# Kernel tuning notes

Measured on AMD Instinct MI355X. Metric: run time of the kernel, lower is better.

## Reference

```python
import jax, jax.numpy as jnp
import numpy as np
from jax import lax

TAU = 2.0     # spikingjelly LIFNode default tau
ALPHA = 4.0   # sigmoid surrogate default alpha

@jax.custom_vjp
def spike(x):
    # heaviside: spikingjelly uses (x >= 0)
    return (x >= 0).astype(x.dtype)

def _spike_fwd(x):
    return spike(x), x

def _spike_bwd(x, g):
    s = jax.nn.sigmoid(ALPHA * x)
    return (g * ALPHA * s * (1.0 - s),)

spike.defvjp(_spike_fwd, _spike_bwd)

def lif(x_seq, v_th):
    """Multi-step LIF: v += (x - v)/tau (decay_input, v_reset=0); hard reset."""
    def step(v, xt):
        v = v + (xt - v) / TAU
        s = spike(v - v_th)
        return (1.0 - s) * v, s
    _, out = lax.scan(step, jnp.zeros_like(x_seq[0]), x_seq)
    return out  # [T,B,C,V] of {0,1}

def conv_bn(x, W, scale, shift):
    # 1x1 Conv1d (no bias) on [T,B,C,V] + eval-mode BatchNorm(s) fused to affine
    y = jnp.einsum('oc,tbcv->tbov', W, x)
    return y * scale[None, None, :, None] + shift[None, None, :, None]

def setup_inputs() -> dict:
    key = jax.random.key(0)
    ks = jax.random.split(key, 16)
    T, B, C, V = 4, 16, 512, 1024
    d = {"x": jax.random.normal(ks[0], (T, B, C, V), jnp.float32)}
    for i, n in enumerate(["q", "k", "v", "p"]):
        d[f"W{n}"] = jax.random.normal(ks[1 + i], (C, C), jnp.float32) * 0.02
        d[f"s{n}"] = 1.0 + 0.1 * jax.random.normal(ks[5 + i], (C,), jnp.float32)
        d[f"b{n}"] = 0.1 * jax.random.normal(ks[9 + i], (C,), jnp.float32)
    return d

def reference(x, Wq, sq, bq, Wk, sk, bk, Wv, sv, bv, Wp, sp, bp):
    T, B, C, V = x.shape
    H = 8
    dh = C // H
    attn_scale = 0.125

    xs = lif(x, 1.0)                              # head_lif, spikes in {0,1}
    q = lif(conv_bn(xs, Wq, sq, bq), 1.0)         # [T,B,C,V]
    k = lif(conv_bn(xs, Wk, sk, bk), 1.0)
    v = lif(conv_bn(xs, Wv, sv, bv), 1.0)

    def to_heads(t):
        # [T,B,C,V] -> [T,B,H,N,dh]  (N = V)
        return t.transpose(0, 1, 3, 2).reshape(T, B, V, H, dh).transpose(0, 1, 3, 2, 4)

    qh, kh, vh = to_heads(q), to_heads(k), to_heads(v)
    kv = jnp.einsum('tbhnd,tbhne->tbhde', kh, vh)            # [T,B,H,dh,dh]
    o = jnp.einsum('tbhnd,tbhde->tbhne', qh, kv) * attn_scale  # [T,B,H,N,dh]
    o = o.transpose(0, 1, 2, 4, 3).reshape(T, B, C, V)       # -> [T,B,C,N]

    a = lif(o, 0.5)                               # attn_lif, v_threshold=0.5
    return conv_bn(a, Wp, sp, bp)                 # [T,B,C,V]
```

## Files before the change

kernel.cpp:

```cpp
#include <hip/hip_runtime.h>
#include <stdint.h>

#define TT 4
#define BB 16
#define CC 512
#define VV 1024
#define OO 1536

typedef __attribute__((ext_vector_type(4)))  int      i32x4;
typedef __attribute__((ext_vector_type(4)))  float    f32x4;
typedef __attribute__((ext_vector_type(16))) uint8_t  u8x16;
typedef __attribute__((ext_vector_type(8)))  uint8_t  u8x8;
typedef __attribute__((ext_vector_type(8)))  int8_t   i8x8;

__device__ __forceinline__ float bf2f(unsigned short u){
  union { unsigned int i; float f; } x; x.i = ((unsigned int)u) << 16; return x.f;
}
__device__ __forceinline__ unsigned short f2bf(float f){
  union { float f; unsigned int i; } x; x.f = f;
  unsigned int u = x.i;
  return (unsigned short)((u + 0x7fffu + ((u >> 16) & 1u)) >> 16);
}

__device__ __forceinline__ void g2lds16(const void* g, void* l){
  __builtin_amdgcn_global_load_lds(
      (const __attribute__((address_space(1))) unsigned int*)g,
      (__attribute__((address_space(3))) unsigned int*)l,
      16, 0, 0);
}

__global__ __launch_bounds__(256) void k_head_lif_prep(
    const float* __restrict__ x, int8_t* __restrict__ xs8,
    const float* __restrict__ Wq, const float* __restrict__ sq, const float* __restrict__ bq,
    const float* __restrict__ Wk, const float* __restrict__ sk, const float* __restrict__ bk,
    const float* __restrict__ Wv, const float* __restrict__ sv, const float* __restrict__ bv,
    const float* __restrict__ Wp, const float* __restrict__ sp,
    int8_t* __restrict__ Wq8, float* __restrict__ scales, float* __restrict__ bias,
    unsigned short* __restrict__ WpT, int* __restrict__ flags)
{
  int bid = blockIdx.x;
  int tid = threadIdx.x;

  if (bid >= 2048) {
    if (bid < 2176) {
      int idx = bid - 2048;
      int lane = tid & 63, wvv = tid >> 6;
      if (idx == 0 && tid < 2) flags[tid] = 0;
      #pragma unroll
      for (int p = 0; p < 3; ++p) {
        int o = idx*12 + p*4 + wvv;
        const float *W, *s, *b; int oo;
        if (o < 512)       { W = Wq; s = sq; b = bq; oo = o; }
        else if (o < 1024) { W = Wk; s = sk; b = bk; oo = o - 512; }
        else               { W = Wv; s = sv; b = bv; oo = o - 1024; }
        float sv_ = s[oo];
        float w[8]; float amax = 0.f;
        #pragma unroll
        for (int j=0;j<8;j++){
          w[j] = W[oo*512 + lane*8 + j] * sv_;
          amax = fmaxf(amax, fabsf(w[j]));
        }
        #pragma unroll
        for (int off=32; off; off>>=1) amax = fmaxf(amax, __shfl_xor(amax, off));
        float scale = (amax > 0.f) ? amax*(1.f/127.f) : 1.f;
        float inv = 1.f/scale;
        i8x8 q;
        #pragma unroll
        for (int j=0;j<8;j++){
          int qi = (int)rintf(w[j]*inv);
          qi = qi > 127 ? 127 : (qi < -127 ? -127 : qi);
          q[j] = (int8_t)qi;
        }
        *(i8x8*)(Wq8 + o*512 + lane*8) = q;
        if (lane == 0){ scales[o] = scale; bias[o] = b[oo]; }
      }
    } else {
      int j0 = (bid - 2176)*1024 + tid*4;
      #pragma unroll
      for (int i=0;i<4;i++){
        int j = j0 + i; int o = j >> 9, c = j & 511;
        WpT[c*512 + o] = f2bf(Wp[j]*sp[o]);
      }
    }
    return;
  }

  int vt = bid & 15, ct = (bid >> 4) & 7, b = bid >> 7;
  int c0 = ct*64, v0 = vt*64;
  __shared__ uint8_t sp_[64][68];
  int cr = tid >> 4;
  int vr = tid & 15;
  float st[4][4];
  #pragma unroll
  for (int i=0;i<4;i++) for (int j=0;j<4;j++) st[i][j]=0.f;
  for (int t=0;t<TT;t++){
    size_t tb = (size_t)t*BB + b;
    const float* xt = x + (tb*CC + c0) * (size_t)VV + v0;
    #pragma unroll
    for (int i=0;i<4;i++){
      const float4 xv = *(const float4*)(xt + (size_t)(cr + i*16)*VV + vr*4);
      const float xe[4] = {xv.x, xv.y, xv.z, xv.w};
      #pragma unroll
      for (int j=0;j<4;j++){
        float vv = st[i][j];
        vv = vv + (xe[j] - vv) * 0.5f;
        bool s = (vv >= 1.0f);
        sp_[cr + i*16][vr*4 + j] = s ? 1 : 0;
        st[i][j] = s ? 0.f : vv;
      }
    }
    __syncthreads();
    int v_loc = tid >> 2;
    int c16 = (tid & 3) * 16;
    u8x16 o0;
    #pragma unroll
    for (int j=0;j<16;j++) o0[j] = sp_[c16 + j][v_loc];
    *(u8x16*)(xs8 + (tb*VV + v0 + v_loc)*(size_t)CC + c0 + c16) = o0;
    __syncthreads();
  }
}

template<int STORE>
__global__ __launch_bounds__(256, 2) void k_gemm_fused(
    const int8_t* __restrict__ xs8, const int8_t* __restrict__ Wq8,
    const float* __restrict__ scales, const float* __restrict__ bias,
    const float* __restrict__ bp, float* __restrict__ outp,
    uint8_t* __restrict__ spk, int* __restrict__ flags)
{
  if (STORE && flags[0] == 0) return;
  int orig = blockIdx.x;
  int tid = threadIdx.x, lane = tid & 63, wv = tid >> 6;

  float bvv = 0.f;
  if (!STORE) bvv = bp[orig & 511];

  int wg = (orig >> 3) + (orig & 7) * 192;
  int ot = wg % 12;
  int r  = wg / 12;
  int vt = r & 7;
  int b  = r >> 3;
  int o0 = ot*128, v0 = vt*128;

  __shared__ __attribute__((aligned(16))) uint8_t lds[81920];

  int wm = wv >> 1, wn = wv & 1;

  const int8_t* Bg = Wq8 + (size_t)o0 * CC;

  {
    int orl = lane >> 5;
    int sl  = lane & 31;
    #pragma unroll
    for (int i=0;i<16;i++){
      int j = wv*16 + i;
      int orow = j*2 + orl;
      int c16 = sl ^ (orow & 7);
      g2lds16(Bg + (size_t)orow*CC + (c16 << 4), lds + j*1024);
    }
  }

  auto STAGE_A = [&](int buf, const int8_t* base, int k0){
    int rl  = lane >> 2;
    int c16 = (lane & 3) ^ ((lane >> 3) & 3);
    #pragma unroll
    for (int i=0;i<2;i++){
      int j = wv*2 + i;
      g2lds16(base + (size_t)(j*16 + rl)*CC + k0 + (c16 << 4),
              lds + 65536 + buf*8192 + j*1024);
    }
  };
  auto READB = [&](int ks, i32x4* dst){
    #pragma unroll
    for (int n=0;n<4;n++){
      int orow = wn*64 + n*16 + (lane & 15);
      int slot = (((ks & 7) << 2) + (lane >> 4)) ^ (lane & 7);
      dst[n] = *(const i32x4*)(lds + orow*512 + (slot << 4));
    }
  };

  i32x4 acc[4][4];
  float st[4][4][4];
  #pragma unroll
  for (int m=0;m<4;m++)
    #pragma unroll
    for (int n=0;n<4;n++){
      acc[m][n] = (i32x4){0,0,0,0};
      #pragma unroll
      for (int j=0;j<4;j++) st[m][n][j] = 0.f;
    }

  float sc[4], bi[4];
  #pragma unroll
  for (int n=0;n<4;n++){
    int og = o0 + wn*64 + n*16 + (lane & 15);
    sc[n] = scales[og];
    bi[n] = bias[og];
  }

  const int8_t* A0 = xs8 + ((size_t)b*VV + v0) * CC;
  STAGE_A(0, A0, 0);

  int anyspike = 0;
  for (int t=0; t<TT; ++t){
    const int8_t* At = xs8 + ((size_t)(t*BB + b)*VV + v0) * CC;
    const int8_t* An = xs8 + ((size_t)((t+1)*BB + b)*VV + v0) * CC;
    #pragma unroll
    for (int ks=0; ks<8; ++ks){
      int g = t*8 + ks;
      int cur = ks & 1;

      if (STORE) {
        __syncthreads();
      } else {
        asm volatile("s_waitcnt vmcnt(0)" ::: "memory");
        __builtin_amdgcn_s_barrier();
      }

      if (!STORE && g < 21) {
        size_t R = (size_t)g*1536 + orig;
        f32x4 val = (f32x4){bvv, bvv, bvv, bvv};
        __builtin_nontemporal_store(val, (f32x4*)(outp + R*1024 + tid*4));
      }

      if (ks < 7)          STAGE_A(cur^1, At, (ks+1)*64);
      else if (t < TT-1)   STAGE_A(cur^1, An, 0);

      const uint8_t* bufA = lds + 65536 + cur*8192;
      i32x4 af[4], bfr[4];
      #pragma unroll
      for (int m=0;m<4;m++){
        int rr = wm*64 + m*16 + (lane & 15);
        int slot = (lane >> 4) ^ ((lane >> 1) & 3);
        af[m] = *(const i32x4*)(bufA + rr*64 + (slot << 4));
      }
      READB(ks, bfr);

      #pragma unroll
      for (int m=0;m<4;m++)
        #pragma unroll
        for (int n=0;n<4;n++)
          acc[m][n] = __builtin_amdgcn_mfma_i32_16x16x64_i8(af[m], bfr[n], acc[m][n], 0,0,0);
    }
    size_t tb = (size_t)t*BB + b;
    #pragma unroll
    for (int m=0;m<4;m++)
      #pragma unroll
      for (int n=0;n<4;n++)
        #pragma unroll
        for (int j=0;j<4;j++){
          float y = (float)acc[m][n][j] * sc[n] + bi[n];
          float vv = st[m][n][j];
          vv = vv + (y - vv) * 0.5f;
          int s = (vv >= 1.0f) ? 1 : 0;
          anyspike |= s;
          st[m][n][j] = s ? 0.f : vv;
          acc[m][n][j] = 0;
          if (STORE){
            int v  = v0 + wm*64 + m*16 + ((lane >> 4) << 2) + j;
            int og = o0 + wn*64 + n*16 + (lane & 15);
            spk[(tb*VV + v)*(size_t)OO + og] = (uint8_t)s;
          }
        }
  }
  if (!STORE){
    if (orig < 512){
      size_t R = 32256 + (size_t)orig;
      f32x4 val = (f32x4){bvv, bvv, bvv, bvv};
      __builtin_nontemporal_store(val, (f32x4*)(outp + R*1024 + tid*4));
    }
    unsigned long long any = __ballot(anyspike != 0);
    if (any != 0ull && lane == 0) atomicOr(flags, 1);
  }
}

__global__ __launch_bounds__(256) void k_kv(const uint8_t* __restrict__ spk,
                                            float* __restrict__ kv,
                                            const int* __restrict__ flags)
{
  if (flags[0] == 0) return;
  int bid = blockIdx.x;
  int h = bid & 7, b = (bid>>3) & 15, t = bid >> 7;
  size_t tb = (size_t)t*BB + b;
  const uint8_t* kb_g = spk + tb*VV*OO + 512  + h*64;
  const uint8_t* vb_g = spk + tb*VV*OO + 1024 + h*64;
  __shared__ __attribute__((aligned(16))) uint8_t kb[16][64];
  __shared__ __attribute__((aligned(16))) uint8_t vb[16][64];
  int tid = threadIdx.x;
  int d = tid >> 2, e0 = (tid & 3) * 16;
  float acc[16];
  #pragma unroll
  for (int i=0;i<16;i++) acc[i]=0.f;
  for (int n0=0;n0<VV;n0+=16){
    int arr = tid >> 7;
    int rr = (tid >> 3) & 15;
    int ch = (tid & 7) * 8;
    u8x8 val = *(const u8x8*)((arr ? vb_g : kb_g) + (size_t)(n0 + rr)*OO + ch);
    *(u8x8*)&(arr ? vb : kb)[rr][ch] = val;
    __syncthreads();
    #pragma unroll
    for (int nn=0;nn<16;nn++){
      if (kb[nn][d]) {
        #pragma unroll
        for (int i=0;i<16;i++) acc[i] += (vb[nn][e0+i] ? 1.0f : 0.0f);
      }
    }
    __syncthreads();
  }
  float* dst = kv + (((tb*8) + h)*64 + d)*(size_t)64 + e0;
  #pragma unroll
  for (int i=0;i<16;i++) dst[i] = acc[i];
}

__global__ __launch_bounds__(256) void k_o_alif(const uint8_t* __restrict__ spk,
                                                const float* __restrict__ kv,
                                                uint8_t* __restrict__ a,
                                                int* __restrict__ flags)
{
  if (flags[0] == 0) return;
  int bid = blockIdx.x;
  int nt = bid & 7, h = (bid>>3) & 7, b = bid >> 6;
  int n0 = nt * 128;
  __shared__ __attribute__((aligned(16))) float kvb[64][64];
  int tid = threadIdx.x;
  int nl = tid >> 1, e0 = (tid & 1) * 32;
  float st[32];
  #pragma unroll
  for (int i=0;i<32;i++) st[i]=0.f;
  int anyA = 0;
  for (int t=0;t<TT;t++){
    size_t tb = (size_t)t*BB + b;
    const f32x4* src = (const f32x4*)(kv + ((tb*8) + h)*(size_t)4096);
    #pragma unroll
    for (int i=0;i<4;i++) ((f32x4*)kvb)[tid + i*256] = src[tid + i*256];
    __syncthreads();
    const uint8_t* qrow = spk + (tb*VV + n0 + nl)*(size_t)OO + h*64;
    float accv[32];
    #pragma unroll
    for (int i=0;i<32;i++) accv[i]=0.f;
    for (int d8=0; d8<8; d8++){
      u8x8 qv = *(const u8x8*)(qrow + d8*8);
      #pragma unroll
      for (int jj=0;jj<8;jj++){
        if (qv[jj]) {
          int dd = d8*8 + jj;
          #pragma unroll
          for (int i=0;i<32;i++) accv[i] += kvb[dd][e0+i];
        }
      }
    }
    uint8_t* arow = a + (tb*VV + n0 + nl)*(size_t)CC + h*64 + e0;
    #pragma unroll
    for (int i=0;i<32;i++){
      float o = accv[i] * 0.125f;
      float vv = st[i];
      vv = vv + (o - vv)*0.5f;
      bool s = (vv >= 0.5f);
      st[i] = s ? 0.f : vv;
      arow[i] = s ? 1 : 0;
      anyA |= (int)s;
    }
    __syncthreads();
  }
  __shared__ int sA;
  if (tid==0) sA=0;
  __syncthreads();
  if (anyA) sA=1;
  __syncthreads();
  if (tid==0 && sA) atomicOr(flags+1, 1);
}

__global__ __launch_bounds__(256) void k_out_add(const uint8_t* __restrict__ a,
                                                 const unsigned short* __restrict__ WpT,
                                                 float* __restrict__ out,
                                                 const int* __restrict__ flags)
{
  if (flags[1] == 0) return;
  int bid = blockIdx.x;
  int vt = bid & 15, b = (bid>>4) & 15, t = bid >> 8;
  size_t tb = (size_t)t*BB + b;
  int v0 = vt*64;
  int tid = threadIdx.x;
  for (int vi=0; vi<64; vi++){
    int v = v0 + vi;
    const uint8_t* av = a + (tb*VV + v)*(size_t)CC;
    for (int c=0;c<CC;c++){
      if (av[c]) {
        #pragma unroll
        for (int i=0;i<2;i++){
          int o = tid + i*256;
          out[((tb*CC) + o)*(size_t)VV + v] += bf2f(WpT[c*512 + o]);
        }
      }
    }
  }
}

extern "C" void kernel_launch(void* const* d_in, const int* in_sizes, int n_in,
                              void* d_out, int out_size, void* d_ws, size_t ws_size,
                              hipStream_t stream)
{
  (void)in_sizes; (void)n_in; (void)out_size;
  const float* x  = (const float*)d_in[0];
  const float* Wq = (const float*)d_in[1];
  const float* sq = (const float*)d_in[2];
  const float* bq = (const float*)d_in[3];
  const float* Wk = (const float*)d_in[4];
  const float* sk = (const float*)d_in[5];
  const float* bk = (const float*)d_in[6];
  const float* Wv = (const float*)d_in[7];
  const float* sv = (const float*)d_in[8];
  const float* bv = (const float*)d_in[9];
  const float* Wp = (const float*)d_in[10];
  const float* sp = (const float*)d_in[11];
  const float* bp = (const float*)d_in[12];
  float* out = (float*)d_out;
  uint8_t* ws = (uint8_t*)d_ws;

  if (ws_size < 177483792ull) return;

  int8_t*         xs8   = (int8_t*)(ws + 0);
  int8_t*         Wq8   = (int8_t*)(ws + 33554432ull);
  float*          scales= (float*)(ws + 34340864ull);
  float*          bias  = (float*)(ws + 34347008ull);
  unsigned short* WpT   = (unsigned short*)(ws + 34353152ull);
  float*          kv    = (float*)(ws + 34877440ull);
  uint8_t*        spk   = (uint8_t*)(ws + 43266048ull);
  uint8_t*        abuf  = (uint8_t*)(ws + 143929344ull);
  int*            flags = (int*)(ws + 177483776ull);

  k_head_lif_prep<<<2432,256,0,stream>>>(x, xs8, Wq,sq,bq, Wk,sk,bk, Wv,sv,bv,
                                         Wp,sp, Wq8, scales, bias, WpT, flags);
  k_gemm_fused<0><<<1536,256,0,stream>>>(xs8, Wq8, scales, bias, bp, out, spk, flags);
  k_gemm_fused<1><<<1536,256,0,stream>>>(xs8, Wq8, scales, bias, bp, out, spk, flags);
  k_kv<<<512,256,0,stream>>>(spk, kv, flags);
  k_o_alif<<<1024,256,0,stream>>>(spk, kv, abuf, flags);
  k_out_add<<<1024,256,0,stream>>>(abuf, WpT, out, flags);
}
```

Before: 96.18 us.

## Give each wave a private A tile to drop per-step block barriers

The A operand staging buffer is changed from a block-shared double buffer into one private single buffer per wave. Each wave now loads its own 64 rows, so the per-k-step __syncthreads/s_barrier is replaced by per-wave vmcnt waits, and the next tile's load is issued after the MFMAs, once the LDS reads have drained. The bias-fill output stores move after the compute and use vmcnt(1) so they do not block the wait. The cost is that waves sharing wm now load duplicate A rows, and single buffering exposes load latency unless other waves hide it.

Result: slower. 103.2 us (+7.3%).

```diff
diff --git a/kernel.cpp b/kernel.cpp
--- a/kernel.cpp
+++ b/kernel.cpp
@@ -159,14 +159,15 @@
     }
   }
 
-  auto STAGE_A = [&](int buf, const int8_t* base, int k0){
+  uint8_t* bufA = lds + 65536 + wv*4096;
+
+  auto STAGE_A = [&](const int8_t* base, int k0){
     int rl  = lane >> 2;
     int c16 = (lane & 3) ^ ((lane >> 3) & 3);
     #pragma unroll
-    for (int i=0;i<2;i++){
-      int j = wv*2 + i;
-      g2lds16(base + (size_t)(j*16 + rl)*CC + k0 + (c16 << 4),
-              lds + 65536 + buf*8192 + j*1024);
+    for (int j=0;j<4;j++){
+      g2lds16(base + (size_t)(wm*64 + j*16 + rl)*CC + k0 + (c16 << 4),
+              bufA + j*1024);
     }
   };
   auto READB = [&](int ks, i32x4* dst){
@@ -198,7 +199,8 @@
   }
 
   const int8_t* A0 = xs8 + ((size_t)b*VV + v0) * CC;
-  STAGE_A(0, A0, 0);
+  STAGE_A(A0, 0);
+  __syncthreads();
 
   int anyspike = 0;
   for (int t=0; t<TT; ++t){
@@ -207,29 +209,18 @@
     #pragma unroll
     for (int ks=0; ks<8; ++ks){
       int g = t*8 + ks;
-      int cur = ks & 1;
-
       if (STORE) {
-        __syncthreads();
+        asm volatile("s_waitcnt vmcnt(0)" ::: "memory");
       } else {
-        asm volatile("s_waitcnt vmcnt(0)" ::: "memory");
-        __builtin_amdgcn_s_barrier();
-      }
-
-      if (!STORE && g < 21) {
-        size_t R = (size_t)g*1536 + orig;
-        f32x4 val = (f32x4){bvv, bvv, bvv, bvv};
-        __builtin_nontemporal_store(val, (f32x4*)(outp + R*1024 + tid*4));
-      }
-
-      if (ks < 7)          STAGE_A(cur^1, At, (ks+1)*64);
-      else if (t < TT-1)   STAGE_A(cur^1, An, 0);
-
-      const uint8_t* bufA = lds + 65536 + cur*8192;
+        bool stored_prev = (g >= 1) && ((g-1 < 21) || (g-1 == 21 && orig < 512));
+        if (stored_prev) asm volatile("s_waitcnt vmcnt(1)" ::: "memory");
+        else             asm volatile("s_waitcnt vmcnt(0)" ::: "memory");
+      }
+
       i32x4 af[4], bfr[4];
       #pragma unroll
       for (int m=0;m<4;m++){
-        int rr = wm*64 + m*16 + (lane & 15);
+        int rr = m*16 + (lane & 15);
         int slot = (lane >> 4) ^ ((lane >> 1) & 3);
         af[m] = *(const i32x4*)(bufA + rr*64 + (slot << 4));
       }
@@ -240,6 +231,22 @@
         #pragma unroll
         for (int n=0;n<4;n++)
           acc[m][n] = __builtin_amdgcn_mfma_i32_16x16x64_i8(af[m], bfr[n], acc[m][n], 0,0,0);
+
+      asm volatile("s_waitcnt lgkmcnt(0)" ::: "memory");
+      if (ks < 7)          STAGE_A(At, (ks+1)*64);
+      else if (t < TT-1)   STAGE_A(An, 0);
+
+      if (!STORE) {
+        if (g < 21) {
+          size_t R = (size_t)g*1536 + orig;
+          f32x4 val = (f32x4){bvv, bvv, bvv, bvv};
+          __builtin_nontemporal_store(val, (f32x4*)(outp + R*1024 + tid*4));
+        } else if (g == 21 && orig < 512) {
+          size_t R = 32256 + (size_t)orig;
+          f32x4 val = (f32x4){bvv, bvv, bvv, bvv};
+          __builtin_nontemporal_store(val, (f32x4*)(outp + R*1024 + tid*4));
+        }
+      }
     }
     size_t tb = (size_t)t*BB + b;
     #pragma unroll
@@ -263,11 +270,6 @@
         }
   }
   if (!STORE){
-    if (orig < 512){
-      size_t R = 32256 + (size_t)orig;
-      f32x4 val = (f32x4){bvv, bvv, bvv, bvv};
-      __builtin_nontemporal_store(val, (f32x4*)(outp + R*1024 + tid*4));
-    }
     unsigned long long any = __ballot(anyspike != 0);
     if (any != 0ull && lane == 0) atomicOr(flags, 1);
   }
```
